# Kernel optimization log

Measured on AMD Instinct MI355X. Metric: run time of the kernel, lower is better.

The kernel has to match this reference:

```python
import jax, jax.numpy as jnp
import numpy as np

THRESH = 1.0
GAMA = 1.0
TAU0 = 0.5

# ZIF surrogate spike: forward hard step, backward triangular surrogate
@jax.custom_vjp
def zif(x):
    return (x > 0).astype(x.dtype)

def _zif_fwd(x):
    return zif(x), x

def _zif_bwd(x, g):
    surr = (1.0 / GAMA) * (1.0 / GAMA) * jnp.clip(GAMA - jnp.abs(x), 0.0, None)
    return (g * surr,)

zif.defvjp(_zif_fwd, _zif_bwd)


def setup_inputs() -> dict:
    key = jax.random.key(0)
    k1, k2, k3, k4, k5 = jax.random.split(key, 5)
    B, T, C, H, W = 32, 8, 128, 32, 32
    red = 4
    x = jax.random.normal(k1, (B, T, C, H, W), dtype=jnp.float32)
    # fc1: Linear(C, C//red); fc2: Linear(C//red, 1); PyTorch default init scale
    s1 = 1.0 / np.sqrt(C)
    s2 = 1.0 / np.sqrt(C // red)
    w1 = jax.random.uniform(k2, (C // red, C), jnp.float32, -s1, s1)
    b1 = jax.random.uniform(k3, (C // red,), jnp.float32, -s1, s1)
    w2 = jax.random.uniform(k4, (1, C // red), jnp.float32, -s2, s2)
    b2 = jax.random.uniform(k5, (1,), jnp.float32, -s2, s2)
    return {"x": x, "w1": w1, "b1": b1, "w2": w2, "b2": b2}


def reference(x, w1, b1, w2, b2):
    B, T, C, H, W = x.shape

    def step(carry, xt):
        mem, tau = carry  # mem: [B,C,H,W], tau: [B,1,1,1]
        mem = mem * tau + xt
        # SE-style gating MLP on channel means
        x_mean = jnp.mean(mem, axis=(-1, -2))          # [B,C]
        embed = jax.nn.relu(x_mean @ w1.T + b1)        # [B,C//r]
        lifp = jax.nn.sigmoid(embed @ w2.T + b2)       # [B,1]
        new_tau = lifp[:, :, None, None]               # [B,1,1,1]
        spike = zif(mem - THRESH)
        mem = (1.0 - spike) * mem
        return (mem, new_tau), spike

    mem0 = jnp.zeros((B, C, H, W), dtype=x.dtype)
    tau0 = jnp.full((B, 1, 1, 1), TAU0, dtype=x.dtype)
    xt = jnp.transpose(x, (1, 0, 2, 3, 4))  # [T,B,C,H,W]
    _, spikes = jax.lax.scan(step, (mem0, tau0), xt)
    return jnp.transpose(spikes, (1, 0, 2, 3, 4))  # [B,T,C,H,W]
```

## Files before the change

### kernel.cpp

```cpp
#include <hip/hip_runtime.h>

typedef float v4f __attribute__((ext_vector_type(4)));

#define NB   32
#define NT   8
#define NC   128
#define NQ   256
#define CRED 32

#define NWORDS (NT * NB * NC * 2)

__device__ unsigned long long g_xw[NWORDS];

__global__ __launch_bounds__(256)
void lif_init() {
    int i = threadIdx.x + blockIdx.x * blockDim.x;
    if (i < NWORDS) g_xw[i] = 0ull;
}

#define LDS_BARRIER() asm volatile("s_waitcnt lgkmcnt(0)\n\ts_barrier" ::: "memory")

__global__ __launch_bounds__(256, 4)
void dynamic_lif(const float* __restrict__ x,
                 const float* __restrict__ w1,
                 const float* __restrict__ b1,
                 const float* __restrict__ w2,
                 const float* __restrict__ b2,
                 float* __restrict__ out)
{
    const int bid = blockIdx.x;
    const int b   = bid >> 5;
    const int c0  = (bid & 31) << 2;
    const int tid = threadIdx.x;
    const int wv  = tid >> 6;
    const int ln  = tid & 63;

    __shared__ double       s_part[4][4];
    __shared__ unsigned int s_w[256];
    __shared__ float        s_tau;

    const v4f* __restrict__ x4 = (const v4f*)x;
    v4f* __restrict__ o4       = (v4f*)out;

    v4f mem[4];
    #pragma unroll
    for (int p = 0; p < 4; ++p) mem[p] = (v4f){0.f, 0.f, 0.f, 0.f};

    float tau = 0.5f;

    v4f xv[4];
    #pragma unroll
    for (int p = 0; p < 4; ++p)
        xv[p] = __builtin_nontemporal_load(x4 + ((b * NT + 0) * NC + c0 + p) * NQ + tid);

    for (int t = 0; t < NT; ++t) {
        double psum[4];
        #pragma unroll
        for (int p = 0; p < 4; ++p) {
            v4f m = mem[p];
            m.x = fmaf(m.x, tau, xv[p].x);
            m.y = fmaf(m.y, tau, xv[p].y);
            m.z = fmaf(m.z, tau, xv[p].z);
            m.w = fmaf(m.w, tau, xv[p].w);
            psum[p] = ((double)m.x + (double)m.y) + ((double)m.z + (double)m.w);
            mem[p] = m;
        }

        #pragma unroll
        for (int p = 0; p < 4; ++p) {
            double s = psum[p];
            #pragma unroll
            for (int off = 32; off > 0; off >>= 1) s += __shfl_down(s, off);
            if (ln == 0) s_part[p][wv] = s;
        }
        LDS_BARRIER();

        if (t == NT - 1) {
            #pragma unroll
            for (int p = 0; p < 4; ++p) {
                v4f m = mem[p];
                v4f sp;
                sp.x = (m.x > 1.0f) ? 1.0f : 0.0f;
                sp.y = (m.y > 1.0f) ? 1.0f : 0.0f;
                sp.z = (m.z > 1.0f) ? 1.0f : 0.0f;
                sp.w = (m.w > 1.0f) ? 1.0f : 0.0f;
                __builtin_nontemporal_store(sp,
                    o4 + ((b * NT + t) * NC + c0 + p) * NQ + tid);
            }
            break;
        }

        if (wv == 0) {
            if (ln < 4) {
                double s = (s_part[ln][0] + s_part[ln][1]) +
                           (s_part[ln][2] + s_part[ln][3]);
                double mean = s * (1.0 / 1024.0);
                unsigned long long bits = __double_as_longlong(mean);
                unsigned long long tag  = ((unsigned long long)(t + 1)) << 32;
                const int base = ((t * NB + b) * NC + c0 + ln) * 2;
                __hip_atomic_store(&g_xw[base + 0], tag | (bits & 0xffffffffull),
                                   __ATOMIC_RELAXED, __HIP_MEMORY_SCOPE_AGENT);
                __hip_atomic_store(&g_xw[base + 1], tag | (bits >> 32),
                                   __ATOMIC_RELAXED, __HIP_MEMORY_SCOPE_AGENT);
            }
            #pragma unroll
            for (int p = 0; p < 4; ++p)
                xv[p] = __builtin_nontemporal_load(
                    x4 + ((b * NT + (t + 1)) * NC + c0 + p) * NQ + tid);
            #pragma unroll
            for (int p = 0; p < 4; ++p) {
                v4f m = mem[p];
                v4f sp;
                sp.x = (m.x > 1.0f) ? 1.0f : 0.0f;
                sp.y = (m.y > 1.0f) ? 1.0f : 0.0f;
                sp.z = (m.z > 1.0f) ? 1.0f : 0.0f;
                sp.w = (m.w > 1.0f) ? 1.0f : 0.0f;
                __builtin_nontemporal_store(sp,
                    o4 + ((b * NT + t) * NC + c0 + p) * NQ + tid);
                m.x = (m.x > 1.0f) ? 0.0f : m.x;
                m.y = (m.y > 1.0f) ? 0.0f : m.y;
                m.z = (m.z > 1.0f) ? 0.0f : m.z;
                m.w = (m.w > 1.0f) ? 0.0f : m.w;
                mem[p] = m;
            }

            {
                const int wbase = (t * NB + b) * NC * 2;
                const unsigned int want = (unsigned int)(t + 1);
                #pragma unroll
                for (int j = 0; j < 4; ++j) {
                    unsigned long long w;
                    for (;;) {
                        w = __hip_atomic_load(&g_xw[wbase + ln + 64 * j],
                                              __ATOMIC_RELAXED,
                                              __HIP_MEMORY_SCOPE_AGENT);
                        if ((unsigned int)(w >> 32) == want) break;
                        __builtin_amdgcn_s_sleep(1);
                    }
                    s_w[ln + 64 * j] = (unsigned int)w;
                }
            }
            asm volatile("s_waitcnt lgkmcnt(0)" ::: "memory");

            double e = 0.0;
            if (ln < CRED) {
                const v4f* __restrict__ w1v = (const v4f*)(w1 + ln * NC);
                double acc = (double)b1[ln];
                #pragma unroll
                for (int q = 0; q < NC / 4; ++q) {
                    v4f wq = w1v[q];
                    #pragma unroll
                    for (int k = 0; k < 4; ++k) {
                        const int c = 4 * q + k;
                        unsigned long long bits =
                            ((unsigned long long)s_w[2 * c + 1] << 32) | s_w[2 * c];
                        double xm = __longlong_as_double(bits);
                        acc += xm * (double)((k == 0) ? wq.x : (k == 1) ? wq.y
                                             : (k == 2) ? wq.z : wq.w);
                    }
                }
                double emb = acc > 0.0 ? acc : 0.0;
                e = emb * (double)w2[ln];
            }
            #pragma unroll
            for (int off = 32; off > 0; off >>= 1) e += __shfl_down(e, off);
            if (ln == 0) {
                double z = e + (double)b2[0];
                s_tau = (float)(1.0 / (1.0 + exp(-z)));
            }
        } else {
            #pragma unroll
            for (int p = 0; p < 4; ++p)
                xv[p] = __builtin_nontemporal_load(
                    x4 + ((b * NT + (t + 1)) * NC + c0 + p) * NQ + tid);
            #pragma unroll
            for (int p = 0; p < 4; ++p) {
                v4f m = mem[p];
                v4f sp;
                sp.x = (m.x > 1.0f) ? 1.0f : 0.0f;
                sp.y = (m.y > 1.0f) ? 1.0f : 0.0f;
                sp.z = (m.z > 1.0f) ? 1.0f : 0.0f;
                sp.w = (m.w > 1.0f) ? 1.0f : 0.0f;
                __builtin_nontemporal_store(sp,
                    o4 + ((b * NT + t) * NC + c0 + p) * NQ + tid);
                m.x = (m.x > 1.0f) ? 0.0f : m.x;
                m.y = (m.y > 1.0f) ? 0.0f : m.y;
                m.z = (m.z > 1.0f) ? 0.0f : m.z;
                m.w = (m.w > 1.0f) ? 0.0f : m.w;
                mem[p] = m;
            }
        }

        LDS_BARRIER();
        tau = s_tau;
    }
}

extern "C" void kernel_launch(void* const* d_in, const int* in_sizes, int n_in,
                              void* d_out, int out_size, void* d_ws, size_t ws_size,
                              hipStream_t stream) {
    const float* x  = (const float*)d_in[0];
    const float* w1 = (const float*)d_in[1];
    const float* b1 = (const float*)d_in[2];
    const float* w2 = (const float*)d_in[3];
    const float* b2 = (const float*)d_in[4];
    float* out      = (float*)d_out;

    hipLaunchKernelGGL(lif_init, dim3((NWORDS + 255) / 256), dim3(256),
                       0, stream);
    hipLaunchKernelGGL(dynamic_lif, dim3(NB * NC / 4), dim3(256), 0, stream,
                       x, w1, b1, w2, b2, out);
}
```

Baseline: 271.4 us.

## Offload wave 0 global loads/stores to other waves and vectorize cross-block poll

Wave 0 handles the cross-block gating MLP, so it no longer loads the next x tile or stores its spike output. Wave 1 prefetches wave 0's x slice into LDS and wave 2 writes wave 0's spikes from LDS, taking global memory traffic off the critical serial path. The polling loop now loads four contiguous tagged words per lane and exits on a wave-wide vote, packing the means directly as 64-bit values in LDS. The cost is extra LDS traffic and more work on waves 1 and 2.

```diff
diff --git a/kernel.cpp b/kernel.cpp
--- a/kernel.cpp
+++ b/kernel.cpp
@@ -35,9 +35,11 @@
     const int wv  = tid >> 6;
     const int ln  = tid & 63;
 
-    __shared__ double       s_part[4][4];
-    __shared__ unsigned int s_w[256];
-    __shared__ float        s_tau;
+    __shared__ double             s_part[4][4];
+    __shared__ v4f                s_xv0[4][64];
+    __shared__ v4f                s_sp0[4][64];
+    __shared__ unsigned long long s_xm[NC];
+    __shared__ float              s_tau;
 
     const v4f* __restrict__ x4 = (const v4f*)x;
     v4f* __restrict__ o4       = (v4f*)out;
@@ -54,6 +56,11 @@
         xv[p] = __builtin_nontemporal_load(x4 + ((b * NT + 0) * NC + c0 + p) * NQ + tid);
 
     for (int t = 0; t < NT; ++t) {
+        if (wv == 0 && t > 0) {
+            #pragma unroll
+            for (int p = 0; p < 4; ++p) xv[p] = s_xv0[p][ln];
+        }
+
         double psum[4];
         #pragma unroll
         for (int p = 0; p < 4; ++p) {
@@ -65,13 +72,30 @@
             psum[p] = ((double)m.x + (double)m.y) + ((double)m.z + (double)m.w);
             mem[p] = m;
         }
-
         #pragma unroll
         for (int p = 0; p < 4; ++p) {
             double s = psum[p];
             #pragma unroll
             for (int off = 32; off > 0; off >>= 1) s += __shfl_down(s, off);
             if (ln == 0) s_part[p][wv] = s;
+        }
+
+        if (t < NT - 1 && wv == 0) {
+            #pragma unroll
+            for (int p = 0; p < 4; ++p) {
+                v4f m = mem[p];
+                v4f sp;
+                sp.x = (m.x > 1.0f) ? 1.0f : 0.0f;
+                sp.y = (m.y > 1.0f) ? 1.0f : 0.0f;
+                sp.z = (m.z > 1.0f) ? 1.0f : 0.0f;
+                sp.w = (m.w > 1.0f) ? 1.0f : 0.0f;
+                s_sp0[p][ln] = sp;
+                m.x = (m.x > 1.0f) ? 0.0f : m.x;
+                m.y = (m.y > 1.0f) ? 0.0f : m.y;
+                m.z = (m.z > 1.0f) ? 0.0f : m.z;
+                m.w = (m.w > 1.0f) ? 0.0f : m.w;
+                mem[p] = m;
+            }
         }
         LDS_BARRIER();
 
@@ -103,45 +127,30 @@
                 __hip_atomic_store(&g_xw[base + 1], tag | (bits >> 32),
                                    __ATOMIC_RELAXED, __HIP_MEMORY_SCOPE_AGENT);
             }
-            #pragma unroll
-            for (int p = 0; p < 4; ++p)
-                xv[p] = __builtin_nontemporal_load(
-                    x4 + ((b * NT + (t + 1)) * NC + c0 + p) * NQ + tid);
-            #pragma unroll
-            for (int p = 0; p < 4; ++p) {
-                v4f m = mem[p];
-                v4f sp;
-                sp.x = (m.x > 1.0f) ? 1.0f : 0.0f;
-                sp.y = (m.y > 1.0f) ? 1.0f : 0.0f;
-                sp.z = (m.z > 1.0f) ? 1.0f : 0.0f;
-                sp.w = (m.w > 1.0f) ? 1.0f : 0.0f;
-                __builtin_nontemporal_store(sp,
-                    o4 + ((b * NT + t) * NC + c0 + p) * NQ + tid);
-                m.x = (m.x > 1.0f) ? 0.0f : m.x;
-                m.y = (m.y > 1.0f) ? 0.0f : m.y;
-                m.z = (m.z > 1.0f) ? 0.0f : m.z;
-                m.w = (m.w > 1.0f) ? 0.0f : m.w;
-                mem[p] = m;
-            }
-
             {
-                const int wbase = (t * NB + b) * NC * 2;
+                const unsigned long long* wp =
+                    g_xw + (t * NB + b) * NC * 2 + 4 * ln;
                 const unsigned int want = (unsigned int)(t + 1);
-                #pragma unroll
-                for (int j = 0; j < 4; ++j) {
-                    unsigned long long w;
-                    for (;;) {
-                        w = __hip_atomic_load(&g_xw[wbase + ln + 64 * j],
-                                              __ATOMIC_RELAXED,
-                                              __HIP_MEMORY_SCOPE_AGENT);
-                        if ((unsigned int)(w >> 32) == want) break;
-                        __builtin_amdgcn_s_sleep(1);
-                    }
-                    s_w[ln + 64 * j] = (unsigned int)w;
+                unsigned long long a0, a1, a2, a3;
+                for (;;) {
+                    a0 = __hip_atomic_load(wp + 0, __ATOMIC_RELAXED,
+                                           __HIP_MEMORY_SCOPE_AGENT);
+                    a1 = __hip_atomic_load(wp + 1, __ATOMIC_RELAXED,
+                                           __HIP_MEMORY_SCOPE_AGENT);
+                    a2 = __hip_atomic_load(wp + 2, __ATOMIC_RELAXED,
+                                           __HIP_MEMORY_SCOPE_AGENT);
+                    a3 = __hip_atomic_load(wp + 3, __ATOMIC_RELAXED,
+                                           __HIP_MEMORY_SCOPE_AGENT);
+                    bool ok = ((unsigned int)(a0 >> 32) == want) &
+                              ((unsigned int)(a1 >> 32) == want) &
+                              ((unsigned int)(a2 >> 32) == want) &
+                              ((unsigned int)(a3 >> 32) == want);
+                    if (__all(ok)) break;
+                    __builtin_amdgcn_s_sleep(1);
                 }
-            }
-            asm volatile("s_waitcnt lgkmcnt(0)" ::: "memory");
-
+                s_xm[2 * ln]     = (a1 << 32) | (a0 & 0xffffffffull);
+                s_xm[2 * ln + 1] = (a3 << 32) | (a2 & 0xffffffffull);
+            }
             double e = 0.0;
             if (ln < CRED) {
                 const v4f* __restrict__ w1v = (const v4f*)(w1 + ln * NC);
@@ -152,9 +161,7 @@
                     #pragma unroll
                     for (int k = 0; k < 4; ++k) {
                         const int c = 4 * q + k;
-                        unsigned long long bits =
-                            ((unsigned long long)s_w[2 * c + 1] << 32) | s_w[2 * c];
-                        double xm = __longlong_as_double(bits);
+                        double xm = __longlong_as_double(s_xm[c]);
                         acc += xm * (double)((k == 0) ? wq.x : (k == 1) ? wq.y
                                              : (k == 2) ? wq.z : wq.w);
                     }
@@ -168,6 +175,62 @@
                 double z = e + (double)b2[0];
                 s_tau = (float)(1.0 / (1.0 + exp(-z)));
             }
+        } else if (wv == 1) {
+            #pragma unroll
+            for (int p = 0; p < 4; ++p)
+                xv[p] = __builtin_nontemporal_load(
+                    x4 + ((b * NT + (t + 1)) * NC + c0 + p) * NQ + tid);
+            v4f t0[4];
+            #pragma unroll
+            for (int p = 0; p < 4; ++p)
+                t0[p] = __builtin_nontemporal_load(
+                    x4 + ((b * NT + (t + 1)) * NC + c0 + p) * NQ + ln);
+            #pragma unroll
+            for (int p = 0; p < 4; ++p) {
+                v4f m = mem[p];
+                v4f sp;
+                sp.x = (m.x > 1.0f) ? 1.0f : 0.0f;
+                sp.y = (m.y > 1.0f) ? 1.0f : 0.0f;
+                sp.z = (m.z > 1.0f) ? 1.0f : 0.0f;
+                sp.w = (m.w > 1.0f) ? 1.0f : 0.0f;
+                __builtin_nontemporal_store(sp,
+                    o4 + ((b * NT + t) * NC + c0 + p) * NQ + tid);
+                m.x = (m.x > 1.0f) ? 0.0f : m.x;
+                m.y = (m.y > 1.0f) ? 0.0f : m.y;
+                m.z = (m.z > 1.0f) ? 0.0f : m.z;
+                m.w = (m.w > 1.0f) ? 0.0f : m.w;
+                mem[p] = m;
+            }
+            #pragma unroll
+            for (int p = 0; p < 4; ++p) s_xv0[p][ln] = t0[p];
+        } else if (wv == 2) {
+            #pragma unroll
+            for (int p = 0; p < 4; ++p)
+                xv[p] = __builtin_nontemporal_load(
+                    x4 + ((b * NT + (t + 1)) * NC + c0 + p) * NQ + tid);
+            v4f sp0[4];
+            #pragma unroll
+            for (int p = 0; p < 4; ++p) sp0[p] = s_sp0[p][ln];
+            #pragma unroll
+            for (int p = 0; p < 4; ++p) {
+                v4f m = mem[p];
+                v4f sp;
+                sp.x = (m.x > 1.0f) ? 1.0f : 0.0f;
+                sp.y = (m.y > 1.0f) ? 1.0f : 0.0f;
+                sp.z = (m.z > 1.0f) ? 1.0f : 0.0f;
+                sp.w = (m.w > 1.0f) ? 1.0f : 0.0f;
+                __builtin_nontemporal_store(sp,
+                    o4 + ((b * NT + t) * NC + c0 + p) * NQ + tid);
+                m.x = (m.x > 1.0f) ? 0.0f : m.x;
+                m.y = (m.y > 1.0f) ? 0.0f : m.y;
+                m.z = (m.z > 1.0f) ? 0.0f : m.z;
+                m.w = (m.w > 1.0f) ? 0.0f : m.w;
+                mem[p] = m;
+            }
+            #pragma unroll
+            for (int p = 0; p < 4; ++p)
+                __builtin_nontemporal_store(sp0[p],
+                    o4 + ((b * NT + t) * NC + c0 + p) * NQ + ln);
         } else {
             #pragma unroll
             for (int p = 0; p < 4; ++p)
```

Result: slower. 307.0 us (+13.1%).
